# Kernel optimization log

Hardware: AMD Instinct MI355X
Metric: run time of the kernel (lower is better)

## Reference

```python
import jax, jax.numpy as jnp
import numpy as np

B, N, DIM = 4, 4096, 1024
HEADS, DFF, WIN = 16, 4096, 128
EPS = 1e-5


def _layernorm(x, w, b):
    mu = jnp.mean(x, axis=-1, keepdims=True)
    var = jnp.mean(jnp.square(x - mu), axis=-1, keepdims=True)
    return (x - mu) * jax.lax.rsqrt(var + EPS) * w + b


def _local_attention(q, k, v, window):
    # q,k,v: (B, h, N, d); non-causal, look_backward=1, look_forward=1
    Bq, h, n, d = q.shape
    nb = n // window
    scale = d ** -0.5
    q = q.reshape(Bq * h, nb, window, d) * scale
    k = k.reshape(Bq * h, nb, window, d)
    v = v.reshape(Bq * h, nb, window, d)

    def look_around(t):  # (BH, nb, w, d) -> (BH, nb, 3w, d)
        tp = jnp.pad(t, ((0, 0), (1, 1), (0, 0), (0, 0)))
        return jnp.concatenate([tp[:, :-2], tp[:, 1:-1], tp[:, 2:]], axis=2)

    kk = look_around(k)
    vv = look_around(v)

    # validity mask for out-of-range look-around buckets
    idx = jnp.arange(n).reshape(nb, window)
    idx_p = jnp.pad(idx, ((1, 1), (0, 0)), constant_values=-1)
    kidx = jnp.concatenate([idx_p[:-2], idx_p[1:-1], idx_p[2:]], axis=1)  # (nb, 3w)
    valid = (kidx >= 0)[None, :, None, :]  # (1, nb, 1, 3w)

    sim = jnp.einsum('bnid,bnjd->bnij', q, kk)  # (BH, nb, w, 3w)
    neg = jnp.finfo(sim.dtype).min
    sim = jnp.where(valid, sim, neg)
    attn = jax.nn.softmax(sim, axis=-1)
    out = jnp.einsum('bnij,bnjd->bnid', attn, vv)
    return out.reshape(Bq, h, n, d)


def setup_inputs() -> dict:
    key = jax.random.key(0)
    ks = jax.random.split(key, 8)
    w = lambda k, shape: jax.random.normal(k, shape, jnp.float32) * 0.02
    return {
        'x': jax.random.normal(ks[0], (B, N, DIM), jnp.float32),
        'ln1_w': jnp.ones((DIM,), jnp.float32), 'ln1_b': jnp.zeros((DIM,), jnp.float32),
        'qkv_w': w(ks[1], (3 * DIM, DIM)), 'qkv_b': jnp.zeros((3 * DIM,), jnp.float32),
        'proj_w': w(ks[2], (DIM, DIM)), 'proj_b': jnp.zeros((DIM,), jnp.float32),
        'ln2_w': jnp.ones((DIM,), jnp.float32), 'ln2_b': jnp.zeros((DIM,), jnp.float32),
        'fc1_w': w(ks[3], (DFF, DIM)), 'fc1_b': jnp.zeros((DFF,), jnp.float32),
        'fc2_w': w(ks[4], (DIM, DFF)), 'fc2_b': jnp.zeros((DIM,), jnp.float32),
    }


def reference(x, ln1_w, ln1_b, qkv_w, qkv_b, proj_w, proj_b, ln2_w, ln2_b, fc1_w, fc1_b, fc2_w, fc2_b):
    Bx, n, C = x.shape
    h = HEADS
    hd = C // h
    x_norm = _layernorm(x, ln1_w, ln1_b)
    qkv = x_norm @ qkv_w.T + qkv_b  # (B, N, 3C)
    qkv = qkv.reshape(Bx, n, 3, h, hd).transpose(2, 0, 3, 1, 4)  # (3, B, h, N, hd)
    q, k, v = qkv[0], qkv[1], qkv[2]
    attn_out = _local_attention(q, k, v, WIN)  # (B, h, N, hd)
    attn_out = attn_out.transpose(0, 2, 1, 3).reshape(Bx, n, C)
    x = x + (attn_out @ proj_w.T + proj_b)
    y = _layernorm(x, ln2_w, ln2_b)
    y = jax.nn.gelu(y @ fc1_w.T + fc1_b, approximate=False)
    x = x + (y @ fc2_w.T + fc2_b)
    return x
```

## Files before the change

### kernel.cpp

```cpp
#include <hip/hip_runtime.h>
#include <math.h>

typedef unsigned short u16;
typedef __attribute__((ext_vector_type(4))) float f32x4;
typedef __attribute__((ext_vector_type(8))) __bf16 bf16x8;
typedef __attribute__((ext_vector_type(8))) u16 u16x8;
typedef __attribute__((ext_vector_type(4))) u16 u16x4;

__device__ __forceinline__ float bf2f(u16 v) {
    unsigned int u = ((unsigned int)v) << 16;
    return __builtin_bit_cast(float, u);
}
__device__ __forceinline__ u16 f2bf(float f) {
    unsigned int x = __builtin_bit_cast(unsigned int, f);
    x += 0x7fffu + ((x >> 16) & 1u);
    return (u16)(x >> 16);
}

__device__ __forceinline__ void load_lds16(const u16* g, u16* l) {
    __builtin_amdgcn_global_load_lds((const __attribute__((address_space(1))) void*)g,
                                     (__attribute__((address_space(3))) void*)l, 16, 0, 0);
}

#define WAIT_VM(N) asm volatile("s_waitcnt vmcnt(" #N ")" ::: "memory")
#define LGKM0_SB() do { asm volatile("s_waitcnt lgkmcnt(0)" ::: "memory"); \
                        __builtin_amdgcn_sched_barrier(0); } while (0)
#define MFMA16(d, x, y) d = __builtin_amdgcn_mfma_f32_16x16x32_bf16(x, y, d, 0, 0, 0)

__global__ __launch_bounds__(256) void cvt_kernel(const float* __restrict__ in,
                                                  u16* __restrict__ out, int n)
{
    const int i = (blockIdx.x * 256 + threadIdx.x) * 4;
    if (i >= n) return;
    const float4 f = *(const float4*)(in + i);
    u16x4 o;
    o[0] = f2bf(f.x); o[1] = f2bf(f.y); o[2] = f2bf(f.z); o[3] = f2bf(f.w);
    *(u16x4*)(out + i) = o;
}

template<int EPI, int RES, bool OF32>
__global__ __launch_bounds__(512, 2) void gemm256(
    const u16* __restrict__ A, const u16* __restrict__ W,
    const float* __restrict__ bias,
    const float* __restrict__ resf, const u16* __restrict__ resb,
    void* __restrict__ O0v, u16* __restrict__ O1, u16* __restrict__ O2,
    int M, int N, int K, int lda, int ldw, int mbase)
{
    __shared__ u16 S[65536];
    const int tid  = threadIdx.x;
    const int w    = tid >> 6;
    const int l    = tid & 63;
    const int colq = l & 15;
    const int quad = l >> 4;
    const int w3   = w & 3;
    const int wm   = (w >> 2) * 128;
    const int wn   = w3 * 64;

    const int nX  = (int)gridDim.x;
    const int nwg = nX * (int)gridDim.y;
    const int did = (int)blockIdx.y * nX + (int)blockIdx.x;
    const int q8  = nwg >> 3;
    const int wg  = (nwg & 7) ? did : ((did & 7) * q8 + (did >> 3));
    const int bm  = wg / nX;
    const int bn  = wg - bm * nX;
    const int m0  = bm * 256, n0 = bn * 256;

    const int rw   = l >> 3;
    const int sseg = ((l & 7) ^ rw) * 8;
    const u16* gA[2][2];
    const u16* gB[2][2];
#pragma unroll
    for (int h = 0; h < 2; ++h)
#pragma unroll
        for (int j = 0; j < 2; ++j) {
            const int rr = w * 16 + j * 8 + rw;
            gA[h][j] = A + (size_t)(m0 + h * 128 + rr) * lda + sseg;
            const int nl = (rr >> 5) * 64 + (h * 2 + ((rr >> 4) & 1)) * 16 + (rr & 15);
            gB[h][j] = W + (size_t)(n0 + nl) * ldw + sseg;
        }
    const int lw = w * 1024;

    const int c0 = (quad * 8) ^ ((colq & 7) << 3);
    const int c1 = c0 ^ 32;

    f32x4 acc[8][4] = {};

#pragma unroll
    for (int h = 0; h < 2; ++h)
#pragma unroll
        for (int j = 0; j < 2; ++j)
            load_lds16(gA[h][j], S + h * 8192 + lw + j * 512);
    load_lds16(gB[0][0], S + 16384 + lw);
    load_lds16(gB[0][1], S + 16384 + lw + 512);
    load_lds16(gB[1][0], S + 16384 + 8192 + lw);
    load_lds16(gB[1][1], S + 16384 + 8192 + lw + 512);
    WAIT_VM(2);
    __builtin_amdgcn_s_barrier();

    const int NT = K >> 6;
    for (int t = 0; t < NT; ++t) {
        u16* Sc = S + ((t & 1) << 15);
        u16* Sn = S + (((t + 1) & 1) << 15);
        const int  kk = (t + 1) << 6;
        const bool pf = (t + 1) < NT;

        bf16x8 aL[4][2], aH[4][2], bL[2][2], bH[2][2];

#pragma unroll
        for (int m = 0; m < 4; ++m) {
            const int rb = (wm + m * 16 + colq) * 64;
            aL[m][0] = *(const bf16x8*)(Sc + rb + c0);
            aL[m][1] = *(const bf16x8*)(Sc + rb + c1);
        }
#pragma unroll
        for (int n = 0; n < 2; ++n) {
            const int rb = 16384 + (w3 * 32 + n * 16 + colq) * 64;
            bL[n][0] = *(const bf16x8*)(Sc + rb + c0);
            bL[n][1] = *(const bf16x8*)(Sc + rb + c1);
        }
        if (pf) {
#pragma unroll
            for (int h = 0; h < 2; ++h)
#pragma unroll
                for (int j = 0; j < 2; ++j)
                    load_lds16(gA[h][j] + kk, Sn + h * 8192 + lw + j * 512);
        }
        __builtin_amdgcn_s_barrier();
        LGKM0_SB();
        __builtin_amdgcn_s_setprio(1);
#pragma unroll
        for (int m = 0; m < 4; ++m)
#pragma unroll
            for (int n = 0; n < 2; ++n) {
                MFMA16(acc[m][n], aL[m][0], bL[n][0]);
                MFMA16(acc[m][n], aL[m][1], bL[n][1]);
            }
        __builtin_amdgcn_s_setprio(0);
        if (pf) { WAIT_VM(4); } else { WAIT_VM(0); }
        __builtin_amdgcn_s_barrier();

#pragma unroll
        for (int n = 0; n < 2; ++n) {
            const int rb = 16384 + 8192 + (w3 * 32 + n * 16 + colq) * 64;
            bH[n][0] = *(const bf16x8*)(Sc + rb + c0);
            bH[n][1] = *(const bf16x8*)(Sc + rb + c1);
        }
        if (pf) {
            load_lds16(gB[0][0] + kk, Sn + 16384 + lw);
            load_lds16(gB[0][1] + kk, Sn + 16384 + lw + 512);
        }
        __builtin_amdgcn_s_barrier();
        LGKM0_SB();
        __builtin_amdgcn_s_setprio(1);
#pragma unroll
        for (int m = 0; m < 4; ++m)
#pragma unroll
            for (int n = 0; n < 2; ++n) {
                MFMA16(acc[m][2 + n], aL[m][0], bH[n][0]);
                MFMA16(acc[m][2 + n], aL[m][1], bH[n][1]);
            }
        __builtin_amdgcn_s_setprio(0);
        __builtin_amdgcn_s_barrier();

#pragma unroll
        for (int m = 0; m < 4; ++m) {
            const int rb = (wm + 64 + m * 16 + colq) * 64;
            aH[m][0] = *(const bf16x8*)(Sc + rb + c0);
            aH[m][1] = *(const bf16x8*)(Sc + rb + c1);
        }
        if (pf) {
            load_lds16(gB[1][0] + kk, Sn + 16384 + 8192 + lw);
            load_lds16(gB[1][1] + kk, Sn + 16384 + 8192 + lw + 512);
        }
        __builtin_amdgcn_s_barrier();
        LGKM0_SB();
        __builtin_amdgcn_s_setprio(1);
#pragma unroll
        for (int m = 0; m < 4; ++m)
#pragma unroll
            for (int n = 0; n < 2; ++n) {
                MFMA16(acc[4 + m][n], aH[m][0], bL[n][0]);
                MFMA16(acc[4 + m][n], aH[m][1], bL[n][1]);
            }
        __builtin_amdgcn_s_setprio(0);
        __builtin_amdgcn_s_barrier();

        __builtin_amdgcn_s_setprio(1);
#pragma unroll
        for (int m = 0; m < 4; ++m)
#pragma unroll
            for (int n = 0; n < 2; ++n) {
                MFMA16(acc[4 + m][2 + n], aH[m][0], bH[n][0]);
                MFMA16(acc[4 + m][2 + n], aH[m][1], bH[n][1]);
            }
        __builtin_amdgcn_s_setprio(0);
        if (pf) { WAIT_VM(2); }
        __builtin_amdgcn_s_barrier();
    }

    if constexpr (EPI == 0) {
        if (n0 >= 2048) {
            __syncthreads();
#pragma unroll
            for (int nf = 0; nf < 4; ++nf) {
                const int cl = wn + nf * 16 + colq;
                const float bz = bias[n0 + cl];
                const int swz = (cl & 7) << 3;
#pragma unroll
                for (int mf = 0; mf < 8; ++mf) {
                    const int rb = wm + mf * 16 + quad * 4;
                    u16x4 pk;
#pragma unroll
                    for (int i = 0; i < 4; ++i) pk[i] = f2bf(acc[mf][nf][i] + bz);
                    *(u16x4*)(S + cl * 256 + (rb ^ swz)) = pk;
                }
            }
            __syncthreads();
            const int cl   = tid >> 1;
            const int c    = n0 + cl;
            const int head = (c >> 6) & 15;
            const int d    = c & 63;
            const int rg0  = mbase + m0;
            const int bh   = (rg0 >> 12) * 16 + head;
            const int half = tid & 1;
            const int swz  = (cl & 7) << 3;
            u16* op = O2 + ((size_t)bh * 64 + d) * 4096 + (rg0 & 4095) + half * 128;
#pragma unroll
            for (int j = 0; j < 16; ++j) {
                const int r0 = half * 128 + j * 8;
                *(u16x8*)(op + j * 8) = *(const u16x8*)(S + cl * 256 + (r0 ^ swz));
            }
            return;
        }
    }
#pragma unroll
    for (int nf = 0; nf < 4; ++nf) {
        const int c = n0 + wn + nf * 16 + colq;
        const float bz = bias ? bias[c] : 0.f;
#pragma unroll
        for (int mf = 0; mf < 8; ++mf) {
#pragma unroll
            for (int i = 0; i < 4; ++i) {
                const int r = m0 + wm + mf * 16 + quad * 4 + i;
                float v = acc[mf][nf][i] + bz;
                if constexpr (EPI == 0) {
                    const int head = (c >> 6) & 15;
                    const int d    = c & 63;
                    const int rg   = mbase + r;
                    const int tt   = rg & 4095;
                    const int bh   = (rg >> 12) * 16 + head;
                    const u16 val = f2bf(v);
                    if (c < 1024) ((u16*)O0v)[((size_t)bh * 4096 + tt) * 64 + d] = val;
                    else          O1[((size_t)bh * 4096 + tt) * 64 + d] = val;
                } else {
                    const size_t idx = (size_t)r * N + c;
                    if constexpr (RES == 1) v += resf[idx];
                    if constexpr (RES == 2) v += bf2f(resb[idx]);
                    if constexpr (EPI == 2) v = 0.5f * v * (1.0f + erff(v * 0.70710678118654752f));
                    if constexpr (OF32) ((float*)O0v)[idx] = v;
                    else                ((u16*)O0v)[idx] = f2bf(v);
                }
            }
        }
    }
}

template<bool F32IN>
__global__ __launch_bounds__(256) void ln_kernel(
    const void* __restrict__ xin, const float* __restrict__ w,
    const float* __restrict__ b, u16* __restrict__ out)
{
    const int wave = threadIdx.x >> 6, lane = threadIdx.x & 63;
    const size_t row = (size_t)blockIdx.x * 4 + wave;
    float v[16];
    if constexpr (F32IN) {
        const float* xr = (const float*)xin + row * 1024 + lane * 16;
#pragma unroll
        for (int j = 0; j < 4; ++j) {
            const float4 f = *(const float4*)(xr + j * 4);
            v[j * 4 + 0] = f.x; v[j * 4 + 1] = f.y; v[j * 4 + 2] = f.z; v[j * 4 + 3] = f.w;
        }
    } else {
        const u16* xr = (const u16*)xin + row * 1024 + lane * 16;
        u16x8 xa = *(const u16x8*)xr;
        u16x8 xb = *(const u16x8*)(xr + 8);
#pragma unroll
        for (int i = 0; i < 8; ++i) { v[i] = bf2f(xa[i]); v[8 + i] = bf2f(xb[i]); }
    }
    float s = 0.f, s2 = 0.f;
#pragma unroll
    for (int i = 0; i < 16; ++i) { s += v[i]; s2 += v[i] * v[i]; }
#pragma unroll
    for (int m = 32; m >= 1; m >>= 1) { s += __shfl_xor(s, m, 64); s2 += __shfl_xor(s2, m, 64); }
    const float mu  = s * (1.0f / 1024.0f);
    const float var = s2 * (1.0f / 1024.0f) - mu * mu;
    const float rs  = rsqrtf(var + 1e-5f);
    const float* wp = w + lane * 16;
    const float* bp = b + lane * 16;
    u16x8 oa, ob;
#pragma unroll
    for (int i = 0; i < 8; ++i) {
        oa[i] = f2bf((v[i]     - mu) * rs * wp[i]     + bp[i]);
        ob[i] = f2bf((v[8 + i] - mu) * rs * wp[8 + i] + bp[8 + i]);
    }
    u16* orow = out + row * 1024 + lane * 16;
    *(u16x8*)orow       = oa;
    *(u16x8*)(orow + 8) = ob;
}

__global__ __launch_bounds__(256, 4) void attn_kernel(
    const u16* __restrict__ Q, const u16* __restrict__ Kb,
    const u16* __restrict__ Vt, u16* __restrict__ out)
{
    __shared__ u16 Ps[4][16 * 200];
    const int tid  = threadIdx.x;
    const int wave = tid >> 6;
    const int lane = tid & 63;
    const int colq = lane & 15;
    const int quad = lane >> 4;

    const int f   = blockIdx.x;
    const int xcd = f & 7;
    const int s8  = f >> 3;
    const int bh  = s8 >> 3;
    const int tb  = (s8 & 7) + 8 * xcd;
    const int qrow0 = tb * 64 + wave * 16;
    const int nb    = tb >> 1;
    const int key0  = nb * 128 - 128;
    const int nt_lo = (nb == 0) ? 8 : 0;
    const int nt_hi = (nb == 31) ? 16 : 24;

    const u16* qp = Q + ((size_t)bh * 4096 + qrow0 + colq) * 64 + quad * 8;
    bf16x8 aq0 = *(const bf16x8*)qp;
    bf16x8 aq1 = *(const bf16x8*)(qp + 32);

    float m_i[4], l_i[4];
    f32x4 o[4] = {};
#pragma unroll
    for (int i = 0; i < 4; ++i) { m_i[i] = -3.0e38f; l_i[i] = 0.f; }

    u16* Psw = &Ps[wave][0];

#pragma unroll
    for (int c = 0; c < 2; ++c) {
        const int lo = (c == 0) ? nt_lo : 12;
        const int hi = (c == 0) ? ((nt_hi < 12) ? nt_hi : 12) : nt_hi;

        f32x4 sc[12];
#pragma unroll
        for (int j = 0; j < 12; ++j) sc[j] = (f32x4){0.f, 0.f, 0.f, 0.f};
#pragma unroll
        for (int j = 0; j < 12; ++j) {
            const int nt = c * 12 + j;
            if (nt >= lo && nt < hi) {
                const u16* kp = Kb + ((size_t)bh * 4096 + key0 + nt * 16 + colq) * 64 + quad * 8;
                bf16x8 b0 = *(const bf16x8*)kp;
                bf16x8 b1 = *(const bf16x8*)(kp + 32);
                f32x4 z = {0.f, 0.f, 0.f, 0.f};
                z = __builtin_amdgcn_mfma_f32_16x16x32_bf16(aq0, b0, z, 0, 0, 0);
                z = __builtin_amdgcn_mfma_f32_16x16x32_bf16(aq1, b1, z, 0, 0, 0);
                sc[j] = z;
            }
        }
        float mc[4];
#pragma unroll
        for (int i = 0; i < 4; ++i) mc[i] = -3.0e38f;
#pragma unroll
        for (int j = 0; j < 12; ++j) {
            const int nt = c * 12 + j;
            if (nt >= lo && nt < hi)
#pragma unroll
                for (int i = 0; i < 4; ++i) mc[i] = fmaxf(mc[i], sc[j][i]);
        }
#pragma unroll
        for (int i = 0; i < 4; ++i)
#pragma unroll
            for (int m = 8; m >= 1; m >>= 1) mc[i] = fmaxf(mc[i], __shfl_xor(mc[i], m, 64));
        float a_i[4], psum[4];
#pragma unroll
        for (int i = 0; i < 4; ++i) {
            const float mn = fmaxf(m_i[i], mc[i]);
            a_i[i] = __expf((m_i[i] - mn) * 0.125f);
            m_i[i] = mn;
            psum[i] = 0.f;
        }
#pragma unroll
        for (int j = 0; j < 12; ++j) {
            const int nt = c * 12 + j;
            if (nt >= lo && nt < hi) {
#pragma unroll
                for (int i = 0; i < 4; ++i) {
                    const float p = __expf((sc[j][i] - m_i[i]) * 0.125f);
                    psum[i] += p;
                    Psw[(quad * 4 + i) * 200 + j * 16 + colq] = f2bf(p);
                }
            }
        }
#pragma unroll
        for (int i = 0; i < 4; ++i)
#pragma unroll
            for (int m = 8; m >= 1; m >>= 1) psum[i] += __shfl_xor(psum[i], m, 64);
#pragma unroll
        for (int i = 0; i < 4; ++i) l_i[i] = l_i[i] * a_i[i] + psum[i];
#pragma unroll
        for (int dt = 0; dt < 4; ++dt)
#pragma unroll
            for (int i = 0; i < 4; ++i) o[dt][i] *= a_i[i];
        const int klo = (lo - c * 12) >> 1;
        const int khi = (hi - c * 12) >> 1;
#pragma unroll
        for (int k6 = 0; k6 < 6; ++k6) {
            if (k6 >= klo && k6 < khi) {
                bf16x8 ap = *(const bf16x8*)(Psw + colq * 200 + k6 * 32 + quad * 8);
                const int kkk = key0 + (c * 6 + k6) * 32 + quad * 8;
#pragma unroll
                for (int dt = 0; dt < 4; ++dt) {
                    const u16* vp = Vt + ((size_t)bh * 64 + dt * 16 + colq) * 4096 + kkk;
                    bf16x8 bv = *(const bf16x8*)vp;
                    o[dt] = __builtin_amdgcn_mfma_f32_16x16x32_bf16(ap, bv, o[dt], 0, 0, 0);
                }
            }
        }
    }

    const int bb = bh >> 4, hh = bh & 15;
#pragma unroll
    for (int i = 0; i < 4; ++i) {
        const float inv = 1.0f / fmaxf(l_i[i], 1e-20f);
        const int t = qrow0 + quad * 4 + i;
        u16* op = out + ((size_t)(bb * 4096 + t)) * 1024 + hh * 64;
#pragma unroll
        for (int dt = 0; dt < 4; ++dt) op[dt * 16 + colq] = f2bf(o[dt][i] * inv);
    }
}

extern "C" void kernel_launch(void* const* d_in, const int* in_sizes, int n_in,
                              void* d_out, int out_size, void* d_ws, size_t ws_size,
                              hipStream_t stream)
{
    const float* x      = (const float*)d_in[0];
    const float* ln1_w  = (const float*)d_in[1];
    const float* ln1_b  = (const float*)d_in[2];
    const float* qkv_w  = (const float*)d_in[3];
    const float* qkv_b  = (const float*)d_in[4];
    const float* proj_w = (const float*)d_in[5];
    const float* proj_b = (const float*)d_in[6];
    const float* ln2_w  = (const float*)d_in[7];
    const float* ln2_b  = (const float*)d_in[8];
    const float* fc1_w  = (const float*)d_in[9];
    const float* fc1_b  = (const float*)d_in[10];
    const float* fc2_w  = (const float*)d_in[11];
    const float* fc2_b  = (const float*)d_in[12];
    float* outp = (float*)d_out;

    if (ws_size < 134217728u) return;
    char* ws = (char*)d_ws;
    u16* R0 = (u16*)(ws);
    u16* R1 = (u16*)(ws + 33554432);
    u16* R2 = (u16*)(ws + 67108864);
    u16* R3 = (u16*)(ws + 100663296);
    u16* attn_o = (u16*)d_out;
    u16* xnc    = (u16*)((char*)d_out + 33554432);

    u16* qkvwb  = R0;
    u16* projwb = R0 + 3145728;
    u16* fc1wb  = R0 + 4194304;
    u16* fc2wb  = R0 + 8388608;
    u16* Qb = R1, *Kb = R2, *Vtb = R3;
    u16* x2 = R1;
    u16* yn = R2;
    u16* hc = R3;

    cvt_kernel<<<3072, 256, 0, stream>>>(qkv_w, qkvwb, 3145728);
    cvt_kernel<<<1024, 256, 0, stream>>>(proj_w, projwb, 1048576);
    cvt_kernel<<<4096, 256, 0, stream>>>(fc1_w, fc1wb, 4194304);
    cvt_kernel<<<4096, 256, 0, stream>>>(fc2_w, fc2wb, 4194304);
    ln_kernel<true><<<4096, 256, 0, stream>>>(x, ln1_w, ln1_b, xnc);
    gemm256<0, 0, false><<<dim3(12, 64), 512, 0, stream>>>(
        xnc, qkvwb, qkv_b, nullptr, nullptr, Qb, Kb, Vtb,
        16384, 3072, 1024, 1024, 1024, 0);
    attn_kernel<<<4096, 256, 0, stream>>>(Qb, Kb, Vtb, attn_o);
    gemm256<1, 1, false><<<dim3(4, 64), 512, 0, stream>>>(
        attn_o, projwb, proj_b, x, nullptr, x2, nullptr, nullptr,
        16384, 1024, 1024, 1024, 1024, 0);
    ln_kernel<false><<<4096, 256, 0, stream>>>(x2, ln2_w, ln2_b, yn);
    for (int c = 0; c < 4; ++c) {
        gemm256<2, 0, false><<<dim3(4, 64), 512, 0, stream>>>(
            yn, fc1wb + (size_t)c * 1048576, fc1_b + c * 1024, nullptr, nullptr,
            hc, nullptr, nullptr, 16384, 1024, 1024, 1024, 1024, 0);
        if (c == 0)
            gemm256<1, 2, true><<<dim3(4, 64), 512, 0, stream>>>(
                hc, fc2wb, fc2_b, nullptr, x2, outp, nullptr, nullptr,
                16384, 1024, 1024, 1024, 4096, 0);
        else
            gemm256<1, 1, true><<<dim3(4, 64), 512, 0, stream>>>(
                hc, fc2wb + c * 1024, nullptr, outp, nullptr, outp, nullptr, nullptr,
                16384, 1024, 1024, 1024, 4096, 0);
    }
}
```

Before: 1.033 ms.

## Restructure MLP into row-chunked full-K GEMMs with narrower fc2 tile, unmask attention

The MLP no longer splits the hidden dimension into four fc1/fc2 pairs that accumulate into the fp32 output. It now splits rows into two halves, runs fc1 over the full 4096 hidden width, then runs a single fc2 with K=4096 using a new 256x128 tile variant (NFR=2), so the output is no longer read and rewritten three extra times. The attention kernel drops its per-tile validity branches: it always computes all score tiles with clamped addresses and then masks scores to a large negative value, and occupancy is raised to 6 blocks. Buffers are reassigned to fit the larger hidden activation. The risks are extra wasted MFMAs on edge buckets and higher register pressure in attention.

```diff
diff --git a/kernel.cpp b/kernel.cpp
--- a/kernel.cpp
+++ b/kernel.cpp
@@ -38,7 +38,7 @@
     *(u16x4*)(out + i) = o;
 }
 
-template<int EPI, int RES, bool OF32>
+template<int EPI, int RES, bool OF32, int NFR>
 __global__ __launch_bounds__(512, 2) void gemm256(
     const u16* __restrict__ A, const u16* __restrict__ W,
     const float* __restrict__ bias,
@@ -46,7 +46,9 @@
     void* __restrict__ O0v, u16* __restrict__ O1, u16* __restrict__ O2,
     int M, int N, int K, int lda, int ldw, int mbase)
 {
-    __shared__ u16 S[65536];
+    constexpr int BBASE = 16384;
+    constexpr int BUFU  = 16384 + NFR * 4096;
+    __shared__ u16 S[2 * BUFU];
     const int tid  = threadIdx.x;
     const int w    = tid >> 6;
     const int l    = tid & 63;
@@ -54,7 +56,7 @@
     const int quad = l >> 4;
     const int w3   = w & 3;
     const int wm   = (w >> 2) * 128;
-    const int wn   = w3 * 64;
+    const int wn   = w3 * (NFR * 16);
 
     const int nX  = (int)gridDim.x;
     const int nwg = nX * (int)gridDim.y;
@@ -63,7 +65,7 @@
     const int wg  = (nwg & 7) ? did : ((did & 7) * q8 + (did >> 3));
     const int bm  = wg / nX;
     const int bn  = wg - bm * nX;
-    const int m0  = bm * 256, n0 = bn * 256;
+    const int m0  = bm * 256, n0 = bn * (NFR * 64);
 
     const int rw   = l >> 3;
     const int sseg = ((l & 7) ^ rw) * 8;
@@ -75,134 +77,202 @@
         for (int j = 0; j < 2; ++j) {
             const int rr = w * 16 + j * 8 + rw;
             gA[h][j] = A + (size_t)(m0 + h * 128 + rr) * lda + sseg;
-            const int nl = (rr >> 5) * 64 + (h * 2 + ((rr >> 4) & 1)) * 16 + (rr & 15);
-            gB[h][j] = W + (size_t)(n0 + nl) * ldw + sseg;
+            if constexpr (NFR == 4) {
+                const int nl = (rr >> 5) * 64 + (h * 2 + ((rr >> 4) & 1)) * 16 + (rr & 15);
+                gB[h][j] = W + (size_t)(n0 + nl) * ldw + sseg;
+            } else if (h == 0) {
+                gB[0][j] = W + (size_t)(n0 + rr) * ldw + sseg;
+            }
         }
     const int lw = w * 1024;
 
     const int c0 = (quad * 8) ^ ((colq & 7) << 3);
     const int c1 = c0 ^ 32;
 
-    f32x4 acc[8][4] = {};
+    f32x4 acc[8][NFR] = {};
 
 #pragma unroll
     for (int h = 0; h < 2; ++h)
 #pragma unroll
         for (int j = 0; j < 2; ++j)
             load_lds16(gA[h][j], S + h * 8192 + lw + j * 512);
-    load_lds16(gB[0][0], S + 16384 + lw);
-    load_lds16(gB[0][1], S + 16384 + lw + 512);
-    load_lds16(gB[1][0], S + 16384 + 8192 + lw);
-    load_lds16(gB[1][1], S + 16384 + 8192 + lw + 512);
-    WAIT_VM(2);
+    load_lds16(gB[0][0], S + BBASE + lw);
+    load_lds16(gB[0][1], S + BBASE + lw + 512);
+    if constexpr (NFR == 4) {
+        load_lds16(gB[1][0], S + BBASE + 8192 + lw);
+        load_lds16(gB[1][1], S + BBASE + 8192 + lw + 512);
+        WAIT_VM(2);
+    } else {
+        WAIT_VM(0);
+    }
     __builtin_amdgcn_s_barrier();
 
     const int NT = K >> 6;
     for (int t = 0; t < NT; ++t) {
-        u16* Sc = S + ((t & 1) << 15);
-        u16* Sn = S + (((t + 1) & 1) << 15);
+        u16* Sc = S + (t & 1) * BUFU;
+        u16* Sn = S + ((t + 1) & 1) * BUFU;
         const int  kk = (t + 1) << 6;
         const bool pf = (t + 1) < NT;
 
-        bf16x8 aL[4][2], aH[4][2], bL[2][2], bH[2][2];
-
-#pragma unroll
-        for (int m = 0; m < 4; ++m) {
-            const int rb = (wm + m * 16 + colq) * 64;
-            aL[m][0] = *(const bf16x8*)(Sc + rb + c0);
-            aL[m][1] = *(const bf16x8*)(Sc + rb + c1);
-        }
-#pragma unroll
-        for (int n = 0; n < 2; ++n) {
-            const int rb = 16384 + (w3 * 32 + n * 16 + colq) * 64;
-            bL[n][0] = *(const bf16x8*)(Sc + rb + c0);
-            bL[n][1] = *(const bf16x8*)(Sc + rb + c1);
-        }
-        if (pf) {
-#pragma unroll
-            for (int h = 0; h < 2; ++h)
-#pragma unroll
-                for (int j = 0; j < 2; ++j)
-                    load_lds16(gA[h][j] + kk, Sn + h * 8192 + lw + j * 512);
-        }
-        __builtin_amdgcn_s_barrier();
-        LGKM0_SB();
-        __builtin_amdgcn_s_setprio(1);
-#pragma unroll
-        for (int m = 0; m < 4; ++m)
+        if constexpr (NFR == 4) {
+            bf16x8 aL[4][2], aH[4][2], bL[2][2], bH[2][2];
+
+#pragma unroll
+            for (int m = 0; m < 4; ++m) {
+                const int rb = (wm + m * 16 + colq) * 64;
+                aL[m][0] = *(const bf16x8*)(Sc + rb + c0);
+                aL[m][1] = *(const bf16x8*)(Sc + rb + c1);
+            }
 #pragma unroll
             for (int n = 0; n < 2; ++n) {
-                MFMA16(acc[m][n], aL[m][0], bL[n][0]);
-                MFMA16(acc[m][n], aL[m][1], bL[n][1]);
-            }
-        __builtin_amdgcn_s_setprio(0);
-        if (pf) { WAIT_VM(4); } else { WAIT_VM(0); }
-        __builtin_amdgcn_s_barrier();
-
-#pragma unroll
-        for (int n = 0; n < 2; ++n) {
-            const int rb = 16384 + 8192 + (w3 * 32 + n * 16 + colq) * 64;
-            bH[n][0] = *(const bf16x8*)(Sc + rb + c0);
-            bH[n][1] = *(const bf16x8*)(Sc + rb + c1);
-        }
-        if (pf) {
-            load_lds16(gB[0][0] + kk, Sn + 16384 + lw);
-            load_lds16(gB[0][1] + kk, Sn + 16384 + lw + 512);
-        }
-        __builtin_amdgcn_s_barrier();
-        LGKM0_SB();
-        __builtin_amdgcn_s_setprio(1);
-#pragma unroll
-        for (int m = 0; m < 4; ++m)
+                const int rb = BBASE + (w3 * 32 + n * 16 + colq) * 64;
+                bL[n][0] = *(const bf16x8*)(Sc + rb + c0);
+                bL[n][1] = *(const bf16x8*)(Sc + rb + c1);
+            }
+            if (pf) {
+#pragma unroll
+                for (int h = 0; h < 2; ++h)
+#pragma unroll
+                    for (int j = 0; j < 2; ++j)
+                        load_lds16(gA[h][j] + kk, Sn + h * 8192 + lw + j * 512);
+            }
+            __builtin_amdgcn_s_barrier();
+            LGKM0_SB();
+            __builtin_amdgcn_s_setprio(1);
+#pragma unroll
+            for (int m = 0; m < 4; ++m)
+#pragma unroll
+                for (int n = 0; n < 2; ++n) {
+                    MFMA16(acc[m][n], aL[m][0], bL[n][0]);
+                    MFMA16(acc[m][n], aL[m][1], bL[n][1]);
+                }
+            __builtin_amdgcn_s_setprio(0);
+            if (pf) { WAIT_VM(4); } else { WAIT_VM(0); }
+            __builtin_amdgcn_s_barrier();
+
 #pragma unroll
             for (int n = 0; n < 2; ++n) {
-                MFMA16(acc[m][2 + n], aL[m][0], bH[n][0]);
-                MFMA16(acc[m][2 + n], aL[m][1], bH[n][1]);
-            }
-        __builtin_amdgcn_s_setprio(0);
-        __builtin_amdgcn_s_barrier();
-
-#pragma unroll
-        for (int m = 0; m < 4; ++m) {
-            const int rb = (wm + 64 + m * 16 + colq) * 64;
-            aH[m][0] = *(const bf16x8*)(Sc + rb + c0);
-            aH[m][1] = *(const bf16x8*)(Sc + rb + c1);
-        }
-        if (pf) {
-            load_lds16(gB[1][0] + kk, Sn + 16384 + 8192 + lw);
-            load_lds16(gB[1][1] + kk, Sn + 16384 + 8192 + lw + 512);
-        }
-        __builtin_amdgcn_s_barrier();
-        LGKM0_SB();
-        __builtin_amdgcn_s_setprio(1);
-#pragma unroll
-        for (int m = 0; m < 4; ++m)
+                const int rb = BBASE + 8192 + (w3 * 32 + n * 16 + colq) * 64;
+                bH[n][0] = *(const bf16x8*)(Sc + rb + c0);
+                bH[n][1] = *(const bf16x8*)(Sc + rb + c1);
+            }
+            if (pf) {
+                load_lds16(gB[0][0] + kk, Sn + BBASE + lw);
+                load_lds16(gB[0][1] + kk, Sn + BBASE + lw + 512);
+            }
+            __builtin_amdgcn_s_barrier();
+            LGKM0_SB();
+            __builtin_amdgcn_s_setprio(1);
+#pragma unroll
+            for (int m = 0; m < 4; ++m)
+#pragma unroll
+                for (int n = 0; n < 2; ++n) {
+                    MFMA16(acc[m][2 + n], aL[m][0], bH[n][0]);
+                    MFMA16(acc[m][2 + n], aL[m][1], bH[n][1]);
+                }
+            __builtin_amdgcn_s_setprio(0);
+            __builtin_amdgcn_s_barrier();
+
+#pragma unroll
+            for (int m = 0; m < 4; ++m) {
+                const int rb = (wm + 64 + m * 16 + colq) * 64;
+                aH[m][0] = *(const bf16x8*)(Sc + rb + c0);
+                aH[m][1] = *(const bf16x8*)(Sc + rb + c1);
+            }
+            if (pf) {
+                load_lds16(gB[1][0] + kk, Sn + BBASE + 8192 + lw);
+                load_lds16(gB[1][1] + kk, Sn + BBASE + 8192 + lw + 512);
+            }
+            __builtin_amdgcn_s_barrier();
+            LGKM0_SB();
+            __builtin_amdgcn_s_setprio(1);
+#pragma unroll
+            for (int m = 0; m < 4; ++m)
+#pragma unroll
+                for (int n = 0; n < 2; ++n) {
+                    MFMA16(acc[4 + m][n], aH[m][0], bL[n][0]);
+                    MFMA16(acc[4 + m][n], aH[m][1], bL[n][1]);
+                }
+            __builtin_amdgcn_s_setprio(0);
+            __builtin_amdgcn_s_barrier();
+
+            __builtin_amdgcn_s_setprio(1);
+#pragma unroll
+            for (int m = 0; m < 4; ++m)
+#pragma unroll
+                for (int n = 0; n < 2; ++n) {
+                    MFMA16(acc[4 + m][2 + n], aH[m][0], bH[n][0]);
+                    MFMA16(acc[4 + m][2 + n], aH[m][1], bH[n][1]);
+                }
+            __builtin_amdgcn_s_setprio(0);
+            if (pf) { WAIT_VM(2); }
+            __builtin_amdgcn_s_barrier();
+        } else {
+            bf16x8 aL[4][2], aH[4][2], bb[2][2];
+
+#pragma unroll
+            for (int m = 0; m < 4; ++m) {
+                const int rb = (wm + m * 16 + colq) * 64;
+                aL[m][0] = *(const bf16x8*)(Sc + rb + c0);
+                aL[m][1] = *(const bf16x8*)(Sc + rb + c1);
+            }
 #pragma unroll
             for (int n = 0; n < 2; ++n) {
-                MFMA16(acc[4 + m][n], aH[m][0], bL[n][0]);
-                MFMA16(acc[4 + m][n], aH[m][1], bL[n][1]);
-            }
-        __builtin_amdgcn_s_setprio(0);
-        __builtin_amdgcn_s_barrier();
-
-        __builtin_amdgcn_s_setprio(1);
-#pragma unroll
-        for (int m = 0; m < 4; ++m)
-#pragma unroll
-            for (int n = 0; n < 2; ++n) {
-                MFMA16(acc[4 + m][2 + n], aH[m][0], bH[n][0]);
-                MFMA16(acc[4 + m][2 + n], aH[m][1], bH[n][1]);
-            }
-        __builtin_amdgcn_s_setprio(0);
-        if (pf) { WAIT_VM(2); }
-        __builtin_amdgcn_s_barrier();
+                const int rb = BBASE + (w3 * 32 + n * 16 + colq) * 64;
+                bb[n][0] = *(const bf16x8*)(Sc + rb + c0);
+                bb[n][1] = *(const bf16x8*)(Sc + rb + c1);
+            }
+            if (pf) {
+#pragma unroll
+                for (int h = 0; h < 2; ++h)
+#pragma unroll
+                    for (int j = 0; j < 2; ++j)
+                        load_lds16(gA[h][j] + kk, Sn + h * 8192 + lw + j * 512);
+            }
+            __builtin_amdgcn_s_barrier();
+            LGKM0_SB();
+            __builtin_amdgcn_s_setprio(1);
+#pragma unroll
+            for (int m = 0; m < 4; ++m)
+#pragma unroll
+                for (int n = 0; n < 2; ++n) {
+                    MFMA16(acc[m][n], aL[m][0], bb[n][0]);
+                    MFMA16(acc[m][n], aL[m][1], bb[n][1]);
+                }
+            __builtin_amdgcn_s_setprio(0);
+            __builtin_amdgcn_s_barrier();
+
+#pragma unroll
+            for (int m = 0; m < 4; ++m) {
+                const int rb = (wm + 64 + m * 16 + colq) * 64;
+                aH[m][0] = *(const bf16x8*)(Sc + rb + c0);
+                aH[m][1] = *(const bf16x8*)(Sc + rb + c1);
+            }
+            if (pf) {
+                load_lds16(gB[0][0] + kk, Sn + BBASE + lw);
+                load_lds16(gB[0][1] + kk, Sn + BBASE + lw + 512);
+            }
+            __builtin_amdgcn_s_barrier();
+            LGKM0_SB();
+            __builtin_amdgcn_s_setprio(1);
+#pragma unroll
+            for (int m = 0; m < 4; ++m)
+#pragma unroll
+                for (int n = 0; n < 2; ++n) {
+                    MFMA16(acc[4 + m][n], aH[m][0], bb[n][0]);
+                    MFMA16(acc[4 + m][n], aH[m][1], bb[n][1]);
+                }
+            __builtin_amdgcn_s_setprio(0);
+            WAIT_VM(0);
+            __builtin_amdgcn_s_barrier();
+        }
     }
 
     if constexpr (EPI == 0) {
         if (n0 >= 2048) {
             __syncthreads();
 #pragma unroll
-            for (int nf = 0; nf < 4; ++nf) {
+            for (int nf = 0; nf < NFR; ++nf) {
                 const int cl = wn + nf * 16 + colq;
                 const float bz = bias[n0 + cl];
                 const int swz = (cl & 7) << 3;
@@ -234,7 +304,7 @@
         }
     }
 #pragma unroll
-    for (int nf = 0; nf < 4; ++nf) {
+    for (int nf = 0; nf < NFR; ++nf) {
         const int c = n0 + wn + nf * 16 + colq;
         const float bz = bias ? bias[c] : 0.f;
 #pragma unroll
@@ -308,7 +378,7 @@
     *(u16x8*)(orow + 8) = ob;
 }
 
-__global__ __launch_bounds__(256, 4) void attn_kernel(
+__global__ __launch_bounds__(256, 6) void attn_kernel(
     const u16* __restrict__ Q, const u16* __restrict__ Kb,
     const u16* __restrict__ Vt, u16* __restrict__ out)
 {
@@ -348,30 +418,32 @@
 
         f32x4 sc[12];
 #pragma unroll
-        for (int j = 0; j < 12; ++j) sc[j] = (f32x4){0.f, 0.f, 0.f, 0.f};
+        for (int j = 0; j < 12; ++j) {
+            const int kr  = key0 + (c * 12 + j) * 16;
+            const int krc = kr < 0 ? 0 : (kr > 4080 ? 4080 : kr);
+            const u16* kp = Kb + ((size_t)bh * 4096 + krc + colq) * 64 + quad * 8;
+            bf16x8 b0 = *(const bf16x8*)kp;
+            bf16x8 b1 = *(const bf16x8*)(kp + 32);
+            f32x4 z = {0.f, 0.f, 0.f, 0.f};
+            z = __builtin_amdgcn_mfma_f32_16x16x32_bf16(aq0, b0, z, 0, 0, 0);
+            z = __builtin_amdgcn_mfma_f32_16x16x32_bf16(aq1, b1, z, 0, 0, 0);
+            sc[j] = z;
+        }
 #pragma unroll
         for (int j = 0; j < 12; ++j) {
             const int nt = c * 12 + j;
-            if (nt >= lo && nt < hi) {
-                const u16* kp = Kb + ((size_t)bh * 4096 + key0 + nt * 16 + colq) * 64 + quad * 8;
-                bf16x8 b0 = *(const bf16x8*)kp;
-                bf16x8 b1 = *(const bf16x8*)(kp + 32);
-                f32x4 z = {0.f, 0.f, 0.f, 0.f};
-                z = __builtin_amdgcn_mfma_f32_16x16x32_bf16(aq0, b0, z, 0, 0, 0);
-                z = __builtin_amdgcn_mfma_f32_16x16x32_bf16(aq1, b1, z, 0, 0, 0);
-                sc[j] = z;
+            if (nt < lo || nt >= hi) {
+#pragma unroll
+                for (int i = 0; i < 4; ++i) sc[j][i] = -3.0e38f;
             }
         }
         float mc[4];
 #pragma unroll
         for (int i = 0; i < 4; ++i) mc[i] = -3.0e38f;
 #pragma unroll
-        for (int j = 0; j < 12; ++j) {
-            const int nt = c * 12 + j;
-            if (nt >= lo && nt < hi)
-#pragma unroll
-                for (int i = 0; i < 4; ++i) mc[i] = fmaxf(mc[i], sc[j][i]);
-        }
+        for (int j = 0; j < 12; ++j)
+#pragma unroll
+            for (int i = 0; i < 4; ++i) mc[i] = fmaxf(mc[i], sc[j][i]);
 #pragma unroll
         for (int i = 0; i < 4; ++i)
 #pragma unroll
@@ -385,17 +457,13 @@
             psum[i] = 0.f;
         }
 #pragma unroll
-        for (int j = 0; j < 12; ++j) {
-            const int nt = c * 12 + j;
-            if (nt >= lo && nt < hi) {
-#pragma unroll
-                for (int i = 0; i < 4; ++i) {
-                    const float p = __expf((sc[j][i] - m_i[i]) * 0.125f);
-                    psum[i] += p;
-                    Psw[(quad * 4 + i) * 200 + j * 16 + colq] = f2bf(p);
-                }
-            }
-        }
+        for (int j = 0; j < 12; ++j)
+#pragma unroll
+            for (int i = 0; i < 4; ++i) {
+                const float p = __expf((sc[j][i] - m_i[i]) * 0.125f);
+                psum[i] += p;
+                Psw[(quad * 4 + i) * 200 + j * 16 + colq] = f2bf(p);
+            }
 #pragma unroll
         for (int i = 0; i < 4; ++i)
 #pragma unroll
@@ -406,19 +474,16 @@
         for (int dt = 0; dt < 4; ++dt)
 #pragma unroll
             for (int i = 0; i < 4; ++i) o[dt][i] *= a_i[i];
-        const int klo = (lo - c * 12) >> 1;
-        const int khi = (hi - c * 12) >> 1;
 #pragma unroll
         for (int k6 = 0; k6 < 6; ++k6) {
-            if (k6 >= klo && k6 < khi) {
-                bf16x8 ap = *(const bf16x8*)(Psw + colq * 200 + k6 * 32 + quad * 8);
-                const int kkk = key0 + (c * 6 + k6) * 32 + quad * 8;
-#pragma unroll
-                for (int dt = 0; dt < 4; ++dt) {
-                    const u16* vp = Vt + ((size_t)bh * 64 + dt * 16 + colq) * 4096 + kkk;
-                    bf16x8 bv = *(const bf16x8*)vp;
-                    o[dt] = __builtin_amdgcn_mfma_f32_16x16x32_bf16(ap, bv, o[dt], 0, 0, 0);
-                }
+            bf16x8 ap = *(const bf16x8*)(Psw + colq * 200 + k6 * 32 + quad * 8);
+            const int kk  = key0 + (c * 6 + k6) * 32 + quad * 8;
+            const int kkc = kk < 0 ? 0 : (kk > 4088 ? 4088 : kk);
+#pragma unroll
+            for (int dt = 0; dt < 4; ++dt) {
+                const u16* vp = Vt + ((size_t)bh * 64 + dt * 16 + colq) * 4096 + kkc;
+                bf16x8 bv = *(const bf16x8*)vp;
+                o[dt] = __builtin_amdgcn_mfma_f32_16x16x32_bf16(ap, bv, o[dt], 0, 0, 0);
             }
         }
     }
@@ -459,8 +524,8 @@
     u16* R1 = (u16*)(ws + 33554432);
     u16* R2 = (u16*)(ws + 67108864);
     u16* R3 = (u16*)(ws + 100663296);
-    u16* attn_o = (u16*)d_out;
-    u16* xnc    = (u16*)((char*)d_out + 33554432);
+    u16* xnc    = (u16*)d_out;
+    u16* attn_o = (u16*)((char*)d_out + 33554432);
 
     u16* qkvwb  = R0;
     u16* projwb = R0 + 3145728;
@@ -468,33 +533,29 @@
     u16* fc2wb  = R0 + 8388608;
     u16* Qb = R1, *Kb = R2, *Vtb = R3;
     u16* x2 = R1;
-    u16* yn = R2;
-    u16* hc = R3;
+    u16* yn = attn_o;
+    u16* hb = R2;
 
     cvt_kernel<<<3072, 256, 0, stream>>>(qkv_w, qkvwb, 3145728);
     cvt_kernel<<<1024, 256, 0, stream>>>(proj_w, projwb, 1048576);
     cvt_kernel<<<4096, 256, 0, stream>>>(fc1_w, fc1wb, 4194304);
     cvt_kernel<<<4096, 256, 0, stream>>>(fc2_w, fc2wb, 4194304);
     ln_kernel<true><<<4096, 256, 0, stream>>>(x, ln1_w, ln1_b, xnc);
-    gemm256<0, 0, false><<<dim3(12, 64), 512, 0, stream>>>(
+    gemm256<0, 0, false, 4><<<dim3(12, 64), 512, 0, stream>>>(
         xnc, qkvwb, qkv_b, nullptr, nullptr, Qb, Kb, Vtb,
         16384, 3072, 1024, 1024, 1024, 0);
     attn_kernel<<<4096, 256, 0, stream>>>(Qb, Kb, Vtb, attn_o);
-    gemm256<1, 1, false><<<dim3(4, 64), 512, 0, stream>>>(
+    gemm256<1, 1, false, 4><<<dim3(4, 64), 512, 0, stream>>>(
         attn_o, projwb, proj_b, x, nullptr, x2, nullptr, nullptr,
         16384, 1024, 1024, 1024, 1024, 0);
     ln_kernel<false><<<4096, 256, 0, stream>>>(x2, ln2_w, ln2_b, yn);
-    for (int c = 0; c < 4; ++c) {
-        gemm256<2, 0, false><<<dim3(4, 64), 512, 0, stream>>>(
-            yn, fc1wb + (size_t)c * 1048576, fc1_b + c * 1024, nullptr, nullptr,
-            hc, nullptr, nullptr, 16384, 1024, 1024, 1024, 1024, 0);
-        if (c == 0)
-            gemm256<1, 2, true><<<dim3(4, 64), 512, 0, stream>>>(
-                hc, fc2wb, fc2_b, nullptr, x2, outp, nullptr, nullptr,
-                16384, 1024, 1024, 1024, 4096, 0);
-        else
-            gemm256<1, 1, true><<<dim3(4, 64), 512, 0, stream>>>(
-                hc, fc2wb + c * 1024, nullptr, outp, nullptr, outp, nullptr, nullptr,
-                16384, 1024, 1024, 1024, 4096, 0);
-    }
-}
+    for (int ci = 0; ci < 2; ++ci) {
+        const size_t off = (size_t)ci * 8192 * 1024;
+        gemm256<2, 0, false, 4><<<dim3(16, 32), 512, 0, stream>>>(
+            yn + off, fc1wb, fc1_b, nullptr, nullptr, hb, nullptr, nullptr,
+            8192, 4096, 1024, 1024, 1024, 0);
+        gemm256<1, 2, true, 2><<<dim3(8, 32), 512, 0, stream>>>(
+            hb, fc2wb, fc2_b, nullptr, x2 + off, outp + off, nullptr, nullptr,
+            8192, 1024, 4096, 4096, 4096, 0);
+    }
+}
```

After: 1.114 ms. +7.8%, slower.

## Rewrite GEMM with BK=32 multi-stage pipeline and restructure MLP chunking

Applied to the files above, without the earlier changes.

Replaces the two-stage BK=64 GEMM main loop with a 3–4 stage BK=32 pipeline, using a new LDS swizzle and a templated N-tile width (256 or 128). The MLP now runs in two row-halves with a full-width fc1 and a K=4096 fc2 that applies the residual directly. Before, it ran four DFF chunks that re-read and re-accumulated the fp32 output. Attention switches to exp2 with a folded log2e scale and raises occupancy bounds, and workspace buffers are reassigned. Deeper prefetch is meant to hide global latency and cut the redundant output traffic, at the cost of more barriers per K-step and higher LDS usage.

```diff
diff --git a/kernel.cpp b/kernel.cpp
--- a/kernel.cpp
+++ b/kernel.cpp
@@ -38,15 +38,18 @@
     *(u16x4*)(out + i) = o;
 }
 
-template<int EPI, int RES, bool OF32>
-__global__ __launch_bounds__(512, 2) void gemm256(
+template<int EPI, int RES, bool OF32, int NFR>
+__global__ __launch_bounds__(512, 2) void gemm32(
     const u16* __restrict__ A, const u16* __restrict__ W,
     const float* __restrict__ bias,
     const float* __restrict__ resf, const u16* __restrict__ resb,
     void* __restrict__ O0v, u16* __restrict__ O1, u16* __restrict__ O2,
     int M, int N, int K, int lda, int ldw, int mbase)
 {
-    __shared__ u16 S[65536];
+    constexpr int STG  = 8192 + NFR * 2048;
+    constexpr int NSTG = (NFR == 4) ? 4 : 3;
+    constexpr int PD   = NSTG - 1;
+    __shared__ u16 S[NSTG * STG];
     const int tid  = threadIdx.x;
     const int w    = tid >> 6;
     const int l    = tid & 63;
@@ -54,7 +57,7 @@
     const int quad = l >> 4;
     const int w3   = w & 3;
     const int wm   = (w >> 2) * 128;
-    const int wn   = w3 * 64;
+    const int wn   = w3 * (NFR * 16);
 
     const int nX  = (int)gridDim.x;
     const int nwg = nX * (int)gridDim.y;
@@ -63,138 +66,87 @@
     const int wg  = (nwg & 7) ? did : ((did & 7) * q8 + (did >> 3));
     const int bm  = wg / nX;
     const int bn  = wg - bm * nX;
-    const int m0  = bm * 256, n0 = bn * 256;
-
-    const int rw   = l >> 3;
-    const int sseg = ((l & 7) ^ rw) * 8;
-    const u16* gA[2][2];
-    const u16* gB[2][2];
-#pragma unroll
-    for (int h = 0; h < 2; ++h)
-#pragma unroll
-        for (int j = 0; j < 2; ++j) {
-            const int rr = w * 16 + j * 8 + rw;
-            gA[h][j] = A + (size_t)(m0 + h * 128 + rr) * lda + sseg;
-            const int nl = (rr >> 5) * 64 + (h * 2 + ((rr >> 4) & 1)) * 16 + (rr & 15);
-            gB[h][j] = W + (size_t)(n0 + nl) * ldw + sseg;
-        }
-    const int lw = w * 1024;
-
-    const int c0 = (quad * 8) ^ ((colq & 7) << 3);
-    const int c1 = c0 ^ 32;
-
-    f32x4 acc[8][4] = {};
-
-#pragma unroll
-    for (int h = 0; h < 2; ++h)
-#pragma unroll
-        for (int j = 0; j < 2; ++j)
-            load_lds16(gA[h][j], S + h * 8192 + lw + j * 512);
-    load_lds16(gB[0][0], S + 16384 + lw);
-    load_lds16(gB[0][1], S + 16384 + lw + 512);
-    load_lds16(gB[1][0], S + 16384 + 8192 + lw);
-    load_lds16(gB[1][1], S + 16384 + 8192 + lw + 512);
-    WAIT_VM(2);
+    const int m0  = bm * 256, n0 = bn * (NFR * 64);
+
+    const int ra  = w * 16 + (l >> 2);
+    const int sa  = (((l & 3) - ((l >> 3) & 3)) & 3) * 8;
+    const u16* gA[2];
+    gA[0] = A + (size_t)(m0 + ra) * lda + sa;
+    gA[1] = A + (size_t)(m0 + 128 + ra) * lda + sa;
+    const u16* gB[2];
+    gB[0] = W + (size_t)(n0 + ra) * ldw + sa;
+    gB[1] = (NFR == 4) ? (W + (size_t)(n0 + 128 + ra) * ldw + sa) : nullptr;
+    const int dw = w * 512;
+
+    const int cs = ((quad + (colq >> 1)) & 3) * 8;
+
+    f32x4 acc[8][NFR] = {};
+
+#pragma unroll
+    for (int s = 0; s < PD; ++s) {
+        const int kk = s << 5;
+        u16* Sp = S + s * STG;
+        load_lds16(gA[0] + kk, Sp + dw);
+        load_lds16(gA[1] + kk, Sp + 4096 + dw);
+        load_lds16(gB[0] + kk, Sp + 8192 + dw);
+        if constexpr (NFR == 4) load_lds16(gB[1] + kk, Sp + 8192 + 4096 + dw);
+    }
+    if constexpr (NFR == 4) { WAIT_VM(8); } else { WAIT_VM(3); }
     __builtin_amdgcn_s_barrier();
 
-    const int NT = K >> 6;
+    const int NT = K >> 5;
     for (int t = 0; t < NT; ++t) {
-        u16* Sc = S + ((t & 1) << 15);
-        u16* Sn = S + (((t + 1) & 1) << 15);
-        const int  kk = (t + 1) << 6;
-        const bool pf = (t + 1) < NT;
-
-        bf16x8 aL[4][2], aH[4][2], bL[2][2], bH[2][2];
-
-#pragma unroll
-        for (int m = 0; m < 4; ++m) {
-            const int rb = (wm + m * 16 + colq) * 64;
-            aL[m][0] = *(const bf16x8*)(Sc + rb + c0);
-            aL[m][1] = *(const bf16x8*)(Sc + rb + c1);
-        }
-#pragma unroll
-        for (int n = 0; n < 2; ++n) {
-            const int rb = 16384 + (w3 * 32 + n * 16 + colq) * 64;
-            bL[n][0] = *(const bf16x8*)(Sc + rb + c0);
-            bL[n][1] = *(const bf16x8*)(Sc + rb + c1);
-        }
+        u16* Sc = S + (t % NSTG) * STG;
+        u16* Sp = S + ((t + PD) % NSTG) * STG;
+        const int  kk = (t + PD) << 5;
+        const bool pf = (t + PD) < NT;
+
+        bf16x8 a[8], p0b0, p0b1;
+#pragma unroll
+        for (int m = 0; m < 8; ++m)
+            a[m] = *(const bf16x8*)(Sc + (wm + m * 16 + colq) * 32 + cs);
+        p0b0 = *(const bf16x8*)(Sc + 8192 + (wn + colq) * 32 + cs);
+        p0b1 = *(const bf16x8*)(Sc + 8192 + (wn + 16 + colq) * 32 + cs);
         if (pf) {
-#pragma unroll
-            for (int h = 0; h < 2; ++h)
-#pragma unroll
-                for (int j = 0; j < 2; ++j)
-                    load_lds16(gA[h][j] + kk, Sn + h * 8192 + lw + j * 512);
+            load_lds16(gA[0] + kk, Sp + dw);
+            load_lds16(gA[1] + kk, Sp + 4096 + dw);
+            if constexpr (NFR == 2) load_lds16(gB[0] + kk, Sp + 8192 + dw);
         }
         __builtin_amdgcn_s_barrier();
         LGKM0_SB();
         __builtin_amdgcn_s_setprio(1);
 #pragma unroll
-        for (int m = 0; m < 4; ++m)
-#pragma unroll
-            for (int n = 0; n < 2; ++n) {
-                MFMA16(acc[m][n], aL[m][0], bL[n][0]);
-                MFMA16(acc[m][n], aL[m][1], bL[n][1]);
-            }
+        for (int m = 0; m < 8; ++m) {
+            MFMA16(acc[m][0], a[m], p0b0);
+            MFMA16(acc[m][1], a[m], p0b1);
+        }
         __builtin_amdgcn_s_setprio(0);
-        if (pf) { WAIT_VM(4); } else { WAIT_VM(0); }
-        __builtin_amdgcn_s_barrier();
-
-#pragma unroll
-        for (int n = 0; n < 2; ++n) {
-            const int rb = 16384 + 8192 + (w3 * 32 + n * 16 + colq) * 64;
-            bH[n][0] = *(const bf16x8*)(Sc + rb + c0);
-            bH[n][1] = *(const bf16x8*)(Sc + rb + c1);
-        }
-        if (pf) {
-            load_lds16(gB[0][0] + kk, Sn + 16384 + lw);
-            load_lds16(gB[0][1] + kk, Sn + 16384 + lw + 512);
-        }
-        __builtin_amdgcn_s_barrier();
-        LGKM0_SB();
-        __builtin_amdgcn_s_setprio(1);
-#pragma unroll
-        for (int m = 0; m < 4; ++m)
-#pragma unroll
-            for (int n = 0; n < 2; ++n) {
-                MFMA16(acc[m][2 + n], aL[m][0], bH[n][0]);
-                MFMA16(acc[m][2 + n], aL[m][1], bH[n][1]);
-            }
-        __builtin_amdgcn_s_setprio(0);
-        __builtin_amdgcn_s_barrier();
-
-#pragma unroll
-        for (int m = 0; m < 4; ++m) {
-            const int rb = (wm + 64 + m * 16 + colq) * 64;
-            aH[m][0] = *(const bf16x8*)(Sc + rb + c0);
-            aH[m][1] = *(const bf16x8*)(Sc + rb + c1);
-        }
-        if (pf) {
-            load_lds16(gB[1][0] + kk, Sn + 16384 + 8192 + lw);
-            load_lds16(gB[1][1] + kk, Sn + 16384 + 8192 + lw + 512);
-        }
-        __builtin_amdgcn_s_barrier();
-        LGKM0_SB();
-        __builtin_amdgcn_s_setprio(1);
-#pragma unroll
-        for (int m = 0; m < 4; ++m)
-#pragma unroll
-            for (int n = 0; n < 2; ++n) {
-                MFMA16(acc[4 + m][n], aH[m][0], bL[n][0]);
-                MFMA16(acc[4 + m][n], aH[m][1], bL[n][1]);
-            }
-        __builtin_amdgcn_s_setprio(0);
-        __builtin_amdgcn_s_barrier();
-
-        __builtin_amdgcn_s_setprio(1);
-#pragma unroll
-        for (int m = 0; m < 4; ++m)
-#pragma unroll
-            for (int n = 0; n < 2; ++n) {
-                MFMA16(acc[4 + m][2 + n], aH[m][0], bH[n][0]);
-                MFMA16(acc[4 + m][2 + n], aH[m][1], bH[n][1]);
-            }
-        __builtin_amdgcn_s_setprio(0);
-        if (pf) { WAIT_VM(2); }
+        if constexpr (NFR == 4) {
+            __builtin_amdgcn_s_barrier();
+
+            bf16x8 p1b0, p1b1;
+            p1b0 = *(const bf16x8*)(Sc + 8192 + (wn + 32 + colq) * 32 + cs);
+            p1b1 = *(const bf16x8*)(Sc + 8192 + (wn + 48 + colq) * 32 + cs);
+            if (pf) {
+                load_lds16(gB[0] + kk, Sp + 8192 + dw);
+                load_lds16(gB[1] + kk, Sp + 8192 + 4096 + dw);
+            }
+            __builtin_amdgcn_s_barrier();
+            LGKM0_SB();
+            __builtin_amdgcn_s_setprio(1);
+#pragma unroll
+            for (int m = 0; m < 8; ++m) {
+                MFMA16(acc[m][2], a[m], p1b0);
+                MFMA16(acc[m][3], a[m], p1b1);
+            }
+            __builtin_amdgcn_s_setprio(0);
+            if ((t + 3) < NT)      { WAIT_VM(8); }
+            else if ((t + 2) < NT) { WAIT_VM(4); }
+            else if ((t + 1) < NT) { WAIT_VM(0); }
+        } else {
+            if ((t + 2) < NT)      { WAIT_VM(3); }
+            else if ((t + 1) < NT) { WAIT_VM(0); }
+        }
         __builtin_amdgcn_s_barrier();
     }
 
@@ -202,7 +154,7 @@
         if (n0 >= 2048) {
             __syncthreads();
 #pragma unroll
-            for (int nf = 0; nf < 4; ++nf) {
+            for (int nf = 0; nf < NFR; ++nf) {
                 const int cl = wn + nf * 16 + colq;
                 const float bz = bias[n0 + cl];
                 const int swz = (cl & 7) << 3;
@@ -234,7 +186,7 @@
         }
     }
 #pragma unroll
-    for (int nf = 0; nf < 4; ++nf) {
+    for (int nf = 0; nf < NFR; ++nf) {
         const int c = n0 + wn + nf * 16 + colq;
         const float bz = bias ? bias[c] : 0.f;
 #pragma unroll
@@ -308,7 +260,7 @@
     *(u16x8*)(orow + 8) = ob;
 }
 
-__global__ __launch_bounds__(256, 4) void attn_kernel(
+__global__ __launch_bounds__(256, 6) void attn_kernel(
     const u16* __restrict__ Q, const u16* __restrict__ Kb,
     const u16* __restrict__ Vt, u16* __restrict__ out)
 {
@@ -318,6 +270,7 @@
     const int lane = tid & 63;
     const int colq = lane & 15;
     const int quad = lane >> 4;
+    const float C2 = 0.18033688011112042f;
 
     const int f   = blockIdx.x;
     const int xcd = f & 7;
@@ -380,7 +333,7 @@
 #pragma unroll
         for (int i = 0; i < 4; ++i) {
             const float mn = fmaxf(m_i[i], mc[i]);
-            a_i[i] = __expf((m_i[i] - mn) * 0.125f);
+            a_i[i] = exp2f((m_i[i] - mn) * C2);
             m_i[i] = mn;
             psum[i] = 0.f;
         }
@@ -390,7 +343,7 @@
             if (nt >= lo && nt < hi) {
 #pragma unroll
                 for (int i = 0; i < 4; ++i) {
-                    const float p = __expf((sc[j][i] - m_i[i]) * 0.125f);
+                    const float p = exp2f((sc[j][i] - m_i[i]) * C2);
                     psum[i] += p;
                     Psw[(quad * 4 + i) * 200 + j * 16 + colq] = f2bf(p);
                 }
@@ -459,8 +412,8 @@
     u16* R1 = (u16*)(ws + 33554432);
     u16* R2 = (u16*)(ws + 67108864);
     u16* R3 = (u16*)(ws + 100663296);
-    u16* attn_o = (u16*)d_out;
-    u16* xnc    = (u16*)((char*)d_out + 33554432);
+    u16* xnc    = (u16*)d_out;
+    u16* attn_o = (u16*)((char*)d_out + 33554432);
 
     u16* qkvwb  = R0;
     u16* projwb = R0 + 3145728;
@@ -468,33 +421,29 @@
     u16* fc2wb  = R0 + 8388608;
     u16* Qb = R1, *Kb = R2, *Vtb = R3;
     u16* x2 = R1;
-    u16* yn = R2;
-    u16* hc = R3;
+    u16* yn = attn_o;
+    u16* hb = R2;
 
     cvt_kernel<<<3072, 256, 0, stream>>>(qkv_w, qkvwb, 3145728);
     cvt_kernel<<<1024, 256, 0, stream>>>(proj_w, projwb, 1048576);
     cvt_kernel<<<4096, 256, 0, stream>>>(fc1_w, fc1wb, 4194304);
     cvt_kernel<<<4096, 256, 0, stream>>>(fc2_w, fc2wb, 4194304);
     ln_kernel<true><<<4096, 256, 0, stream>>>(x, ln1_w, ln1_b, xnc);
-    gemm256<0, 0, false><<<dim3(12, 64), 512, 0, stream>>>(
+    gemm32<0, 0, false, 4><<<dim3(12, 64), 512, 0, stream>>>(
         xnc, qkvwb, qkv_b, nullptr, nullptr, Qb, Kb, Vtb,
         16384, 3072, 1024, 1024, 1024, 0);
     attn_kernel<<<4096, 256, 0, stream>>>(Qb, Kb, Vtb, attn_o);
-    gemm256<1, 1, false><<<dim3(4, 64), 512, 0, stream>>>(
+    gemm32<1, 1, false, 4><<<dim3(4, 64), 512, 0, stream>>>(
         attn_o, projwb, proj_b, x, nullptr, x2, nullptr, nullptr,
         16384, 1024, 1024, 1024, 1024, 0);
     ln_kernel<false><<<4096, 256, 0, stream>>>(x2, ln2_w, ln2_b, yn);
-    for (int c = 0; c < 4; ++c) {
-        gemm256<2, 0, false><<<dim3(4, 64), 512, 0, stream>>>(
-            yn, fc1wb + (size_t)c * 1048576, fc1_b + c * 1024, nullptr, nullptr,
-            hc, nullptr, nullptr, 16384, 1024, 1024, 1024, 1024, 0);
-        if (c == 0)
-            gemm256<1, 2, true><<<dim3(4, 64), 512, 0, stream>>>(
-                hc, fc2wb, fc2_b, nullptr, x2, outp, nullptr, nullptr,
-                16384, 1024, 1024, 1024, 4096, 0);
-        else
-            gemm256<1, 1, true><<<dim3(4, 64), 512, 0, stream>>>(
-                hc, fc2wb + c * 1024, nullptr, outp, nullptr, outp, nullptr, nullptr,
-                16384, 1024, 1024, 1024, 4096, 0);
-    }
-}
+    for (int ci = 0; ci < 2; ++ci) {
+        const size_t off = (size_t)ci * 8192 * 1024;
+        gemm32<2, 0, false, 4><<<dim3(16, 32), 512, 0, stream>>>(
+            yn + off, fc1wb, fc1_b, nullptr, nullptr, hb, nullptr, nullptr,
+            8192, 4096, 1024, 1024, 1024, 0);
+        gemm32<1, 2, true, 2><<<dim3(8, 32), 512, 0, stream>>>(
+            hb, fc2wb, fc2_b, nullptr, x2 + off, outp + off, nullptr, nullptr,
+            8192, 1024, 4096, 4096, 4096, 0);
+    }
+}
```

Result: slower. 1.119 ms (+8.2%).
